# Kernel tuning notes

Hardware: AMD Instinct MI355X
Metric: run time of the kernel (lower is better)

The kernel has to match this reference:

```python
import jax, jax.numpy as jnp
import numpy as np

# SMPL kinematic tree, first 22 joints (root has parent -1)
PARENTS = [-1, 0, 0, 0, 1, 2, 3, 4, 5, 6, 7, 8, 9, 9, 9, 12, 13, 14, 16, 17, 18, 19]
B, L, J = 64, 2048, 22


def axis_angle_to_matrix(aa):
    """aa: (..., 3) axis-angle -> (..., 3, 3) rotation matrix (Rodrigues)."""
    sq = jnp.sum(aa * aa, axis=-1, keepdims=True)
    angle = jnp.sqrt(sq + 1e-12)
    axis = aa / angle
    x, y, z = axis[..., 0], axis[..., 1], axis[..., 2]
    ang = angle[..., 0]
    c, s = jnp.cos(ang), jnp.sin(ang)
    t = 1.0 - c
    R = jnp.stack([
        t * x * x + c,     t * x * y - s * z, t * x * z + s * y,
        t * x * y + s * z, t * y * y + c,     t * y * z - s * x,
        t * x * z - s * y, t * y * z + s * x, t * z * z + c,
    ], axis=-1)
    return R.reshape(aa.shape[:-1] + (3, 3))


def get_TRS(rotmat, pos):
    """rotmat (...,3,3), pos (...,3) -> homogeneous (...,4,4)."""
    top = jnp.concatenate([rotmat, pos[..., :, None]], axis=-1)  # (...,3,4)
    bottom = jnp.broadcast_to(
        jnp.array([0.0, 0.0, 0.0, 1.0], rotmat.dtype), top.shape[:-2] + (1, 4))
    return jnp.concatenate([top, bottom], axis=-2)


def forward_kinematics(mat, parents):
    """mat: (B,L,J,4,4) local transforms -> global transforms via parent chain."""
    out = [mat[:, :, 0]]
    for j in range(1, mat.shape[2]):
        out.append(out[parents[j]] @ mat[:, :, j])
    return jnp.stack(out, axis=2)


def setup_inputs() -> dict:
    key = jax.random.key(0)
    ks = jax.random.split(key, 6)
    return {
        "body_pose": 0.3 * jax.random.normal(ks[0], (B, L, 63), jnp.float32),
        "betas": jax.random.normal(ks[1], (B, L, 10), jnp.float32),
        "global_orient": 0.3 * jax.random.normal(ks[2], (B, L, 3), jnp.float32),
        "transl": jax.random.normal(ks[3], (B, L, 3), jnp.float32),
        "J_template": jax.random.normal(ks[4], (J, 3), jnp.float32),
        "J_shapedirs": 0.01 * jax.random.normal(ks[5], (J, 3, 10), jnp.float32),
    }


def reference(body_pose, betas, global_orient, transl, J_template, J_shapedirs):
    Bm, Lm = body_pose.shape[:2]
    # (B,L,22,3) axis-angle: global orient + 21 body joints
    aa = jnp.concatenate([global_orient, body_pose], axis=-1).reshape(Bm, Lm, -1, 3)
    rotmat = axis_angle_to_matrix(aa)                                  # (B,L,22,3,3)
    skeleton = J_template[None, None] + jnp.einsum('blk,jck->bljc', betas, J_shapedirs)
    # local offsets: child - parent, root keeps its own position (+ transl)
    parent_idx = jnp.array([0] + PARENTS[1:])
    local = skeleton - skeleton[:, :, parent_idx]
    local = local.at[:, :, 0].set(skeleton[:, :, 0] + transl)
    mat = get_TRS(rotmat, local)                                       # (B,L,22,4,4)
    fk_mat = forward_kinematics(mat, PARENTS)                          # (B,L,22,4,4)
    joints = fk_mat[..., :3, 3]                                        # (B,L,22,3)
    return joints
```

## Files before the change

### kernel.cpp

```cpp
#include <hip/hip_runtime.h>

#define NT 128
#define NJ 22

struct X9 { float r[9]; float t[3]; };

__device__ __forceinline__ void rodrigues(float ax, float ay, float az, float* R) {
    float sq   = ax*ax + ay*ay + az*az + 1e-12f;
    float rinv = rsqrtf(sq);
    float ang  = sq * rinv;
    float s, c;
    __sincosf(ang, &s, &c);
    float x = ax*rinv, y = ay*rinv, z = az*rinv;
    float t = 1.0f - c;
    R[0] = t*x*x + c;   R[1] = t*x*y - s*z; R[2] = t*x*z + s*y;
    R[3] = t*x*y + s*z; R[4] = t*y*y + c;   R[5] = t*y*z - s*x;
    R[6] = t*x*z - s*y; R[7] = t*y*z + s*x; R[8] = t*z*z + c;
}

__device__ __forceinline__ void local_pos(int j, const float* bt,
                                          const float* LT, const float* LD,
                                          float* lt) {
    #pragma unroll
    for (int c = 0; c < 3; ++c) {
        float v = LT[j*3 + c];
        #pragma unroll
        for (int k = 0; k < 10; ++k)
            v = fmaf(bt[k], LD[(j*3 + c)*10 + k], v);
        lt[c] = v;
    }
}

template<int J>
__device__ __forceinline__ X9 step(const X9& gp, const float* bp, const float* bt,
                                   const float* LT, const float* LD, float* outp) {
    float R[9];
    rodrigues(bp[(J-1)*3 + 0], bp[(J-1)*3 + 1], bp[(J-1)*3 + 2], R);
    float lt[3];
    local_pos(J, bt, LT, LD, lt);
    X9 g;
    #pragma unroll
    for (int r = 0; r < 3; ++r) {
        #pragma unroll
        for (int c = 0; c < 3; ++c)
            g.r[r*3+c] = fmaf(gp.r[r*3+0], R[c],
                         fmaf(gp.r[r*3+1], R[3+c],
                              gp.r[r*3+2] * R[6+c]));
        g.t[r] = fmaf(gp.r[r*3+0], lt[0],
                 fmaf(gp.r[r*3+1], lt[1],
                 fmaf(gp.r[r*3+2], lt[2], gp.t[r])));
    }
    outp[J*3+0] = g.t[0]; outp[J*3+1] = g.t[1]; outp[J*3+2] = g.t[2];
    return g;
}

__global__ __launch_bounds__(NT) void fk_joints_kernel(
    const float* __restrict__ body_pose,
    const float* __restrict__ betas,
    const float* __restrict__ global_orient,
    const float* __restrict__ transl,
    const float* __restrict__ J_template,
    const float* __restrict__ J_shapedirs,
    float* __restrict__ out)
{
    __shared__ float s_bp[NT*63];
    __shared__ float s_bt[NT*10];
    __shared__ float s_go[NT*3];
    __shared__ float s_tr[NT*3];
    __shared__ float s_LT[NJ*3];
    __shared__ float s_LD[NJ*3*10];

    const int tid = threadIdx.x;
    const long long s0 = (long long)blockIdx.x * NT;

    {
        const float4* src = reinterpret_cast<const float4*>(body_pose + s0*63);
        float4* dst = reinterpret_cast<float4*>(s_bp);
        #pragma unroll 4
        for (int i = tid; i < NT*63/4; i += NT) dst[i] = src[i];
    }
    {
        const float4* src = reinterpret_cast<const float4*>(betas + s0*10);
        float4* dst = reinterpret_cast<float4*>(s_bt);
        for (int i = tid; i < NT*10/4; i += NT) dst[i] = src[i];
    }
    {
        const float4* src = reinterpret_cast<const float4*>(global_orient + s0*3);
        float4* dst = reinterpret_cast<float4*>(s_go);
        if (tid < NT*3/4) dst[tid] = src[tid];
    }
    {
        const float4* src = reinterpret_cast<const float4*>(transl + s0*3);
        float4* dst = reinterpret_cast<float4*>(s_tr);
        if (tid < NT*3/4) dst[tid] = src[tid];
    }

    const int P[NJ] = {0,0,0,0,1,2,3,4,5,6,7,8,9,9,9,12,13,14,16,17,18,19};
    for (int i = tid; i < NJ*3; i += NT) {
        int j = i/3, c = i - j*3;
        float v = J_template[i];
        if (j) v -= J_template[P[j]*3 + c];
        s_LT[i] = v;
    }
    for (int i = tid; i < NJ*30; i += NT) {
        int jc = i/10, k = i - jc*10;
        int j = jc/3,  c = jc - j*3;
        float v = J_shapedirs[i];
        if (j) v -= J_shapedirs[(P[j]*3 + c)*10 + k];
        s_LD[i] = v;
    }
    __syncthreads();

    float bt[10];
    #pragma unroll
    for (int k = 0; k < 10; ++k) bt[k] = s_bt[tid*10 + k];

    const float* bp = &s_bp[tid*63];
    float* outp = out + (s0 + tid) * (NJ*3);

    X9 g0;
    rodrigues(s_go[tid*3+0], s_go[tid*3+1], s_go[tid*3+2], g0.r);
    {
        float lt0[3];
        local_pos(0, bt, s_LT, s_LD, lt0);
        g0.t[0] = lt0[0] + s_tr[tid*3+0];
        g0.t[1] = lt0[1] + s_tr[tid*3+1];
        g0.t[2] = lt0[2] + s_tr[tid*3+2];
        outp[0] = g0.t[0]; outp[1] = g0.t[1]; outp[2] = g0.t[2];
    }

    X9 g;
    g = step<1 >(g0, bp, bt, s_LT, s_LD, outp);
    g = step<4 >(g,  bp, bt, s_LT, s_LD, outp);
    g = step<7 >(g,  bp, bt, s_LT, s_LD, outp);
    g = step<10>(g,  bp, bt, s_LT, s_LD, outp);
    g = step<2 >(g0, bp, bt, s_LT, s_LD, outp);
    g = step<5 >(g,  bp, bt, s_LT, s_LD, outp);
    g = step<8 >(g,  bp, bt, s_LT, s_LD, outp);
    g = step<11>(g,  bp, bt, s_LT, s_LD, outp);
    g = step<3 >(g0, bp, bt, s_LT, s_LD, outp);
    g = step<6 >(g,  bp, bt, s_LT, s_LD, outp);
    X9 g9 = step<9>(g, bp, bt, s_LT, s_LD, outp);
    g = step<12>(g9, bp, bt, s_LT, s_LD, outp);
    g = step<15>(g,  bp, bt, s_LT, s_LD, outp);
    g = step<13>(g9, bp, bt, s_LT, s_LD, outp);
    g = step<16>(g,  bp, bt, s_LT, s_LD, outp);
    g = step<18>(g,  bp, bt, s_LT, s_LD, outp);
    g = step<20>(g,  bp, bt, s_LT, s_LD, outp);
    g = step<14>(g9, bp, bt, s_LT, s_LD, outp);
    g = step<17>(g,  bp, bt, s_LT, s_LD, outp);
    g = step<19>(g,  bp, bt, s_LT, s_LD, outp);
    g = step<21>(g,  bp, bt, s_LT, s_LD, outp);
}

extern "C" void kernel_launch(void* const* d_in, const int* in_sizes, int n_in,
                              void* d_out, int out_size, void* d_ws, size_t ws_size,
                              hipStream_t stream) {
    const float* body_pose     = (const float*)d_in[0];
    const float* betas         = (const float*)d_in[1];
    const float* global_orient = (const float*)d_in[2];
    const float* transl        = (const float*)d_in[3];
    const float* J_template    = (const float*)d_in[4];
    const float* J_shapedirs   = (const float*)d_in[5];
    float* out = (float*)d_out;

    const int S = in_sizes[0] / 63;
    const int blocks = S / NT;

    hipLaunchKernelGGL(fk_joints_kernel, dim3(blocks), dim3(NT), 0, stream,
                       body_pose, betas, global_orient, transl,
                       J_template, J_shapedirs, out);
}
```

Measured before the change: 36.03 us.

## Stage joint outputs in shared memory and write coalesced float4 stores

Each thread now writes its computed joint positions back into its own shared-memory body_pose slot (and the root into s_go) instead of scattering stride-66 global stores. After a block barrier, the whole block emits the output tile with coalesced float4 stores. The shape-direction table is also padded to 12 floats per row so it can be read with float4 LDS loads. The cost is an extra barrier plus per-element index math (a division by 66) in the store loop.

Result: no change. 35.68 us (-1.0%).

```diff
diff --git a/kernel.cpp b/kernel.cpp
--- a/kernel.cpp
+++ b/kernel.cpp
@@ -19,25 +19,30 @@
 }
 
 __device__ __forceinline__ void local_pos(int j, const float* bt,
-                                          const float* LT, const float* LD,
+                                          const float* LT, const float4* LD4,
                                           float* lt) {
     #pragma unroll
     for (int c = 0; c < 3; ++c) {
         float v = LT[j*3 + c];
-        #pragma unroll
-        for (int k = 0; k < 10; ++k)
-            v = fmaf(bt[k], LD[(j*3 + c)*10 + k], v);
+        const float4 a0 = LD4[(j*3 + c)*3 + 0];
+        const float4 a1 = LD4[(j*3 + c)*3 + 1];
+        const float4 a2 = LD4[(j*3 + c)*3 + 2];
+        v = fmaf(bt[0], a0.x, v); v = fmaf(bt[1], a0.y, v);
+        v = fmaf(bt[2], a0.z, v); v = fmaf(bt[3], a0.w, v);
+        v = fmaf(bt[4], a1.x, v); v = fmaf(bt[5], a1.y, v);
+        v = fmaf(bt[6], a1.z, v); v = fmaf(bt[7], a1.w, v);
+        v = fmaf(bt[8], a2.x, v); v = fmaf(bt[9], a2.y, v);
         lt[c] = v;
     }
 }
 
 template<int J>
-__device__ __forceinline__ X9 step(const X9& gp, const float* bp, const float* bt,
-                                   const float* LT, const float* LD, float* outp) {
+__device__ __forceinline__ X9 step(const X9& gp, float* bp, const float* bt,
+                                   const float* LT, const float4* LD4) {
     float R[9];
     rodrigues(bp[(J-1)*3 + 0], bp[(J-1)*3 + 1], bp[(J-1)*3 + 2], R);
     float lt[3];
-    local_pos(J, bt, LT, LD, lt);
+    local_pos(J, bt, LT, LD4, lt);
     X9 g;
     #pragma unroll
     for (int r = 0; r < 3; ++r) {
@@ -50,7 +55,7 @@
                  fmaf(gp.r[r*3+1], lt[1],
                  fmaf(gp.r[r*3+2], lt[2], gp.t[r])));
     }
-    outp[J*3+0] = g.t[0]; outp[J*3+1] = g.t[1]; outp[J*3+2] = g.t[2];
+    bp[(J-1)*3+0] = g.t[0]; bp[(J-1)*3+1] = g.t[1]; bp[(J-1)*3+2] = g.t[2];
     return g;
 }
 
@@ -63,12 +68,12 @@
     const float* __restrict__ J_shapedirs,
     float* __restrict__ out)
 {
-    __shared__ float s_bp[NT*63];
-    __shared__ float s_bt[NT*10];
-    __shared__ float s_go[NT*3];
-    __shared__ float s_tr[NT*3];
-    __shared__ float s_LT[NJ*3];
-    __shared__ float s_LD[NJ*3*10];
+    __shared__ float  s_bp[NT*63];
+    __shared__ float  s_bt[NT*10];
+    __shared__ float  s_go[NT*3];
+    __shared__ float  s_tr[NT*3];
+    __shared__ float  s_LT[NJ*3];
+    __shared__ float4 s_LD4[NJ*3*3];
 
     const int tid = threadIdx.x;
     const long long s0 = (long long)blockIdx.x * NT;
@@ -96,18 +101,21 @@
     }
 
     const int P[NJ] = {0,0,0,0,1,2,3,4,5,6,7,8,9,9,9,12,13,14,16,17,18,19};
+    float* s_LD = reinterpret_cast<float*>(s_LD4);
     for (int i = tid; i < NJ*3; i += NT) {
         int j = i/3, c = i - j*3;
         float v = J_template[i];
         if (j) v -= J_template[P[j]*3 + c];
         s_LT[i] = v;
+        s_LD[i*12 + 10] = 0.0f;
+        s_LD[i*12 + 11] = 0.0f;
     }
     for (int i = tid; i < NJ*30; i += NT) {
         int jc = i/10, k = i - jc*10;
         int j = jc/3,  c = jc - j*3;
         float v = J_shapedirs[i];
         if (j) v -= J_shapedirs[(P[j]*3 + c)*10 + k];
-        s_LD[i] = v;
+        s_LD[jc*12 + k] = v;
     }
     __syncthreads();
 
@@ -115,42 +123,60 @@
     #pragma unroll
     for (int k = 0; k < 10; ++k) bt[k] = s_bt[tid*10 + k];
 
-    const float* bp = &s_bp[tid*63];
-    float* outp = out + (s0 + tid) * (NJ*3);
+    float* bp = &s_bp[tid*63];
 
     X9 g0;
     rodrigues(s_go[tid*3+0], s_go[tid*3+1], s_go[tid*3+2], g0.r);
     {
         float lt0[3];
-        local_pos(0, bt, s_LT, s_LD, lt0);
+        local_pos(0, bt, s_LT, s_LD4, lt0);
         g0.t[0] = lt0[0] + s_tr[tid*3+0];
         g0.t[1] = lt0[1] + s_tr[tid*3+1];
         g0.t[2] = lt0[2] + s_tr[tid*3+2];
-        outp[0] = g0.t[0]; outp[1] = g0.t[1]; outp[2] = g0.t[2];
+        s_go[tid*3+0] = g0.t[0]; s_go[tid*3+1] = g0.t[1]; s_go[tid*3+2] = g0.t[2];
     }
 
     X9 g;
-    g = step<1 >(g0, bp, bt, s_LT, s_LD, outp);
-    g = step<4 >(g,  bp, bt, s_LT, s_LD, outp);
-    g = step<7 >(g,  bp, bt, s_LT, s_LD, outp);
-    g = step<10>(g,  bp, bt, s_LT, s_LD, outp);
-    g = step<2 >(g0, bp, bt, s_LT, s_LD, outp);
-    g = step<5 >(g,  bp, bt, s_LT, s_LD, outp);
-    g = step<8 >(g,  bp, bt, s_LT, s_LD, outp);
-    g = step<11>(g,  bp, bt, s_LT, s_LD, outp);
-    g = step<3 >(g0, bp, bt, s_LT, s_LD, outp);
-    g = step<6 >(g,  bp, bt, s_LT, s_LD, outp);
-    X9 g9 = step<9>(g, bp, bt, s_LT, s_LD, outp);
-    g = step<12>(g9, bp, bt, s_LT, s_LD, outp);
-    g = step<15>(g,  bp, bt, s_LT, s_LD, outp);
-    g = step<13>(g9, bp, bt, s_LT, s_LD, outp);
-    g = step<16>(g,  bp, bt, s_LT, s_LD, outp);
-    g = step<18>(g,  bp, bt, s_LT, s_LD, outp);
-    g = step<20>(g,  bp, bt, s_LT, s_LD, outp);
-    g = step<14>(g9, bp, bt, s_LT, s_LD, outp);
-    g = step<17>(g,  bp, bt, s_LT, s_LD, outp);
-    g = step<19>(g,  bp, bt, s_LT, s_LD, outp);
-    g = step<21>(g,  bp, bt, s_LT, s_LD, outp);
+    g = step<1 >(g0, bp, bt, s_LT, s_LD4);
+    g = step<4 >(g,  bp, bt, s_LT, s_LD4);
+    g = step<7 >(g,  bp, bt, s_LT, s_LD4);
+    g = step<10>(g,  bp, bt, s_LT, s_LD4);
+    g = step<2 >(g0, bp, bt, s_LT, s_LD4);
+    g = step<5 >(g,  bp, bt, s_LT, s_LD4);
+    g = step<8 >(g,  bp, bt, s_LT, s_LD4);
+    g = step<11>(g,  bp, bt, s_LT, s_LD4);
+    g = step<3 >(g0, bp, bt, s_LT, s_LD4);
+    g = step<6 >(g,  bp, bt, s_LT, s_LD4);
+    X9 g9 = step<9>(g, bp, bt, s_LT, s_LD4);
+    g = step<12>(g9, bp, bt, s_LT, s_LD4);
+    g = step<15>(g,  bp, bt, s_LT, s_LD4);
+    g = step<13>(g9, bp, bt, s_LT, s_LD4);
+    g = step<16>(g,  bp, bt, s_LT, s_LD4);
+    g = step<18>(g,  bp, bt, s_LT, s_LD4);
+    g = step<20>(g,  bp, bt, s_LT, s_LD4);
+    g = step<14>(g9, bp, bt, s_LT, s_LD4);
+    g = step<17>(g,  bp, bt, s_LT, s_LD4);
+    g = step<19>(g,  bp, bt, s_LT, s_LD4);
+    g = step<21>(g,  bp, bt, s_LT, s_LD4);
+
+    __syncthreads();
+
+    {
+        float4* dst = reinterpret_cast<float4*>(out + s0 * (NJ*3));
+        const int TOT4 = NT*NJ*3/4;
+        for (int i = tid; i < TOT4; i += NT) {
+            const int f0 = i*4;
+            float v[4];
+            #pragma unroll
+            for (int q = 0; q < 4; ++q) {
+                int f = f0 + q;
+                int s = f / 66;
+                int r = f - s*66;
+                v[q] = (r < 3) ? s_go[s*3 + r] : s_bp[s*63 + (r - 3)];
+            }
+            dst[i] = make_float4(v[0], v[1], v[2], v[3]);
+        }
+    }
 }
 
 extern "C" void kernel_launch(void* const* d_in, const int* in_sizes, int n_in,
```
